# Kernel optimization log

Measured on AMD Instinct MI355X. Metric: run time of the kernel, lower is better.

Reference implementation:

```python
import jax, jax.numpy as jnp
import numpy as np

B, T, U, N, K, H, O = 64, 800, 64, 64, 10, 512, 121
CLIP_LSTM, CLIP_OUT = 10.0, 100.0


def setup_inputs() -> dict:
    key = jax.random.key(0)
    ks = jax.random.split(key, 16)
    s = 0.08
    return {
        "strokes": jax.random.normal(ks[0], (B, T, 3), jnp.float32),
        "transcriptions": jax.random.uniform(ks[1], (B, U, N), jnp.float32),
        "W0": jax.random.normal(ks[2], (3 + N, 4 * H), jnp.float32) * s,
        "R0": jax.random.normal(ks[3], (H, 4 * H), jnp.float32) * s,
        "b0": jnp.zeros((4 * H,), jnp.float32),
        "Wd": jax.random.normal(ks[4], (H, 3 * K), jnp.float32) * 0.01,
        "bd": jnp.zeros((3 * K,), jnp.float32),
        "W1": jax.random.normal(ks[5], (H + N + 3, 4 * H), jnp.float32) * s,
        "R1": jax.random.normal(ks[6], (H, 4 * H), jnp.float32) * s,
        "b1": jnp.zeros((4 * H,), jnp.float32),
        "W2": jax.random.normal(ks[7], (H + N + 3, 4 * H), jnp.float32) * s,
        "R2": jax.random.normal(ks[8], (H, 4 * H), jnp.float32) * s,
        "b2": jnp.zeros((4 * H,), jnp.float32),
        "Wo": jax.random.normal(ks[9], (3 * H, O), jnp.float32) * s,
        "bo": jnp.zeros((O,), jnp.float32),
    }


def _lstm_step(h, c, z):
    i, f, g, o = jnp.split(z, 4, axis=-1)
    c2 = jax.nn.sigmoid(f) * c + jax.nn.sigmoid(i) * jnp.tanh(g)
    h2 = jax.nn.sigmoid(o) * jnp.tanh(c2)
    return h2, c2


def _lstm_layer(x_seq, W, R, b):
    # x_seq: [T, B, D] -> hidden sequence [T, B, H]
    xz = jnp.einsum('tbd,dh->tbh', x_seq, W) + b  # precompute input projections

    def step(carry, xz_t):
        h, c = carry
        h2, c2 = _lstm_step(h, c, xz_t + h @ R)
        return (h2, c2), h2

    z0 = jnp.zeros((x_seq.shape[1], R.shape[0]), x_seq.dtype)
    _, hs = jax.lax.scan(step, (z0, z0), xz)
    return hs


def _make_clipper(cv):
    @jax.custom_vjp
    def f(y):
        return y
    f.defvjp(lambda y: (y, None), lambda _, dy: (jnp.clip(dy, -cv, cv),))
    return f


_clip_lstm = _make_clipper(CLIP_LSTM)
_clip_out = _make_clipper(CLIP_OUT)


def _forward(strokes, transcriptions, W0, R0, b0, Wd, bd, W1, R1, b1, W2, R2, b2, Wo, bo):
    idx = jnp.arange(1, U + 2, dtype=strokes.dtype)  # enumerated char positions [U+1]
    x_t = jnp.swapaxes(strokes, 0, 1)  # [T, B, 3]

    def step(carry, x):
        w, kappa, h, c = carry
        z = jnp.concatenate([x, w], axis=-1) @ W0 + h @ R0 + b0
        h2, c2 = _lstm_step(h, c, z)
        y = jnp.exp(h2 @ Wd + bd).reshape(-1, 3, K)  # [B, 3, K]
        alpha, beta, dk = y[:, 0], y[:, 1], y[:, 2]
        kappa2 = kappa + dk  # [B, K]
        # Gaussian window over U+1 positions, summed over K mixtures
        phi = alpha[..., None] * jnp.exp(-beta[..., None] * (kappa2[..., None] - idx) ** 2)
        wfull = phi.sum(axis=1)  # [B, U+1]
        att = jnp.argmax(wfull, axis=-1).astype(strokes.dtype)  # [B]
        w2 = jnp.einsum('bu,bun->bn', wfull[:, :U], transcriptions)  # soft window [B, N]
        return (w2, kappa2, h2, c2), (h2, w2, att)

    zf = lambda d: jnp.zeros((B, d), strokes.dtype)
    init = (zf(N), zf(K), zf(H), zf(H))
    _, (h0_seq, w_seq, att_seq) = jax.lax.scan(step, init, x_t)

    x1 = jnp.concatenate([_clip_lstm(h0_seq), w_seq, x_t], axis=-1)  # [T, B, H+N+3]
    h1_seq = _lstm_layer(x1, W1, R1, b1)
    x2 = jnp.concatenate([_clip_lstm(h1_seq), w_seq, x_t], axis=-1)
    h2_seq = _lstm_layer(x2, W2, R2, b2)
    hall = jnp.concatenate([h0_seq, h1_seq, h2_seq], axis=-1)  # [T, B, 3H]
    out = _clip_out(hall @ Wo + bo)
    return jnp.swapaxes(out, 0, 1), jnp.swapaxes(att_seq, 0, 1)  # [B,T,O], [B,T]


def reference(strokes, transcriptions, W0, R0, b0, Wd, bd, W1, R1, b1, W2, R2, b2, Wo, bo):
    return _forward(strokes, transcriptions, W0, R0, b0, Wd, bd, W1, R1, b1, W2, R2, b2, Wo, bo)
```

## Files before the change

### kernel.cpp

```cpp
#include <hip/hip_runtime.h>

#define B_   64
#define T_   800
#define U_   64
#define N_   64
#define KMIX 10
#define H_   512
#define O_   121
#define C4_  2048

#define NB_L0  64
#define NB_L1  64
#define NB_L2  64
#define NB_OUT 8
#define NB_ATT 4
#define NBLK  (NB_L0 + NB_L1 + NB_L2 + NB_OUT + NB_ATT)
#define NTHR  512
#define RING  8
#define RB    (RING - 1)
#define FS    8

#define AL(pp) __hip_atomic_load((pp), __ATOMIC_RELAXED, __HIP_MEMORY_SCOPE_AGENT)

struct Params {
  const float* strokes; const float* transcr;
  const float* W0; const float* b0;
  const float* bd;
  const float* W1; const float* b1;
  const float* W2; const float* b2;
  const float* bo;
  const float4* PR0; const float4* PW0w;
  const float4* PH1; const float4* PR1; const float4* PW1w;
  const float4* PH2; const float4* PR2; const float4* PW2w;
  const float4* PWo; const float4* PWd;
  float* h0r; float* h1r; float* h2r;
  float* wr;
  int *h0f, *h1f, *h2f, *wfl, *outf;
  float* outp; float* attp;
};

__device__ __forceinline__ float sigf(float x) { return 1.0f / (1.0f + expf(-x)); }

__device__ __forceinline__ double f32q(double x) {
  double ax = fabs(x);
  if (ax >= 0x1p-126) return (double)(float)x;
  return rint(x * 0x1p149) * 0x1p-149;
}

__device__ __forceinline__ void cstoref(float* p, float v) {
  __hip_atomic_store(p, v, __ATOMIC_RELAXED, __HIP_MEMORY_SCOPE_AGENT);
}

__device__ __forceinline__ int* FP(int* arr, int tt, int bq) {
  return arr + ((size_t)tt * 8 + bq) * FS;
}
__device__ __forceinline__ void waitflag(const int* f, int target) {
  while (__hip_atomic_load(f, __ATOMIC_RELAXED, __HIP_MEMORY_SCOPE_AGENT) < target)
    __builtin_amdgcn_s_sleep(1);
}
__device__ __forceinline__ void postflag(int* f) {
  __hip_atomic_fetch_add(f, 1, __ATOMIC_RELAXED, __HIP_MEMORY_SCOPE_AGENT);
}

__device__ __forceinline__ void stage4k(float* dstL, const float* src, int t) {
  const double* s = (const double*)src;
  double v0 = AL(s + t), v1 = AL(s + 512 + t), v2 = AL(s + 1024 + t), v3 = AL(s + 1536 + t);
  double* d = (double*)dstL;
  d[t] = v0; d[512 + t] = v1; d[1024 + t] = v2; d[1536 + t] = v3;
}
__device__ __forceinline__ void stage4k2(float* d1, const float* s1,
                                         float* d2, const float* s2, int t) {
  const double* a = (const double*)s1;
  const double* b = (const double*)s2;
  double a0 = AL(a + t), a1 = AL(a + 512 + t), a2 = AL(a + 1024 + t), a3 = AL(a + 1536 + t);
  double b0 = AL(b + t), b1 = AL(b + 512 + t), b2 = AL(b + 1024 + t), b3 = AL(b + 1536 + t);
  double* dA = (double*)d1; dA[t] = a0; dA[512 + t] = a1; dA[1024 + t] = a2; dA[1536 + t] = a3;
  double* dB = (double*)d2; dB[t] = b0; dB[512 + t] = b1; dB[1024 + t] = b2; dB[1536 + t] = b3;
}
__device__ __forceinline__ void stage512(float* dstL, const float* src, int t) {
  if (t < 256) {
    double v = AL((const double*)src + t);
    ((double*)dstL)[t] = v;
  }
}

__device__ __forceinline__ void dot4gl(const float* Xl,
                                       const float4* __restrict__ W,
                                       int k4, int col, float acc[4]) {
  const float4* X = (const float4*)Xl;
  #pragma unroll 2
  for (int kk = 0; kk < k4; ++kk) {
    float4 xv = X[kk];
    #pragma unroll
    for (int g = 0; g < 4; ++g) {
      float4 wv = W[kk * C4_ + g * H_ + col];
      acc[g] = fmaf(xv.x, wv.x, acc[g]);
      acc[g] = fmaf(xv.y, wv.y, acc[g]);
      acc[g] = fmaf(xv.z, wv.z, acc[g]);
      acc[g] = fmaf(xv.w, wv.w, acc[g]);
    }
  }
}

__device__ __forceinline__ float dot1l(const float* Xl,
                                       const float4* __restrict__ W,
                                       int k4, int stride) {
  const float4* X = (const float4*)Xl;
  float a = 0.0f;
  #pragma unroll 4
  for (int kk = 0; kk < k4; ++kk) {
    float4 xv = X[kk];
    float4 wv = W[kk * stride];
    a = fmaf(xv.x, wv.x, a); a = fmaf(xv.y, wv.y, a);
    a = fmaf(xv.z, wv.z, a); a = fmaf(xv.w, wv.w, a);
  }
  return a;
}

__global__ void pack_k(const float* __restrict__ src, float* __restrict__ dst,
                       int K, int C, int ld) {
  int idx = blockIdx.x * 256 + threadIdx.x;
  if (idx >= K * C) return;
  int k = idx / C, c = idx - k * C;
  dst[(size_t)(k >> 2) * C * 4 + (size_t)c * 4 + (k & 3)] = src[(size_t)k * ld + c];
}

__global__ __launch_bounds__(NTHR, 2)
void net_kernel(Params p) {
  const int q = blockIdx.x;
  const int t = threadIdx.x;

  __shared__ float  s_buf[12288];
  __shared__ float  s_y[16][32];
  __shared__ float  s_k2[16][10];
  __shared__ float  s_kap[16][10];
  __shared__ double s_wf[16][66];

  if (q < NB_L0) {
    const int bq = q >> 3, colg = q & 7;
    const int bl = t >> 6, cl = t & 63;
    const int b = bq * 8 + bl, col = colg * 64 + cl;
    float* sh = s_buf;
    float* sw = s_buf + 4096;
    float creg = 0.0f;
    for (int i = 0; i < T_; ++i) {
      if (t == 0) {
        if (i >= 1) waitflag(FP(p.h0f, i - 1, bq), 8);
        if (i >= 8) waitflag(FP(p.outf, i - 8, bq), 1);
      }
      __syncthreads();
      const int slp = (i - 1) & RB;
      stage4k(sh, &p.h0r[((size_t)slp * B_ + bq * 8) * H_], t);
      float acc[4];
      const float* xs = &p.strokes[(b * T_ + i) * 3];
      float x0 = xs[0], x1 = xs[1], x2 = xs[2];
      #pragma unroll
      for (int g = 0; g < 4; ++g) {
        int cg = g * H_ + col;
        acc[g] = p.b0[cg] + x0 * p.W0[cg] + x1 * p.W0[C4_ + cg] + x2 * p.W0[2 * C4_ + cg];
      }
      __syncthreads();
      dot4gl(sh + bl * H_, p.PR0, H_ / 4, col, acc);
      if (t == 0 && i >= 1) waitflag(FP(p.wfl, i - 1, bq), 1);
      __syncthreads();
      stage512(sw, &p.wr[((size_t)slp * B_ + bq * 8) * N_], t);
      __syncthreads();
      dot4gl(sw + bl * N_, p.PW0w, N_ / 4, col, acc);
      float cn = sigf(acc[1]) * creg + sigf(acc[0]) * tanhf(acc[2]);
      float hn = sigf(acc[3]) * tanhf(cn);
      creg = cn;
      cstoref(&p.h0r[((size_t)(i & RB) * B_ + b) * H_ + col], hn);
      __syncthreads();
      if (t == 0) postflag(FP(p.h0f, i, bq));
    }
  } else if (q < NB_L0 + NB_L1) {
    const int qq = q - NB_L0;
    const int bq = qq >> 3, colg = qq & 7;
    const int bl = t >> 6, cl = t & 63;
    const int b = bq * 8 + bl, col = colg * 64 + cl;
    float* sh0 = s_buf;
    float* sh1 = s_buf + 4096;
    float* sw  = s_buf + 8192;
    float creg = 0.0f;
    for (int tt = 0; tt < T_; ++tt) {
      if (t == 0) {
        waitflag(FP(p.h0f, tt, bq), 8);
        if (tt >= 1) waitflag(FP(p.h1f, tt - 1, bq), 8);
        if (tt >= 7) waitflag(FP(p.outf, tt - 7, bq), 1);
      }
      __syncthreads();
      const int sl = tt & RB, slp = (tt - 1) & RB;
      stage4k2(sh0, &p.h0r[((size_t)sl * B_ + bq * 8) * H_],
               sh1, &p.h1r[((size_t)slp * B_ + bq * 8) * H_], t);
      float acc[4];
      const float* xs = &p.strokes[(b * T_ + tt) * 3];
      float x0 = xs[0], x1 = xs[1], x2 = xs[2];
      #pragma unroll
      for (int g = 0; g < 4; ++g) {
        int cg = g * H_ + col;
        acc[g] = p.b1[cg] + x0 * p.W1[576 * C4_ + cg] + x1 * p.W1[577 * C4_ + cg]
                          + x2 * p.W1[578 * C4_ + cg];
      }
      __syncthreads();
      dot4gl(sh0 + bl * H_, p.PH1, H_ / 4, col, acc);
      dot4gl(sh1 + bl * H_, p.PR1, H_ / 4, col, acc);
      if (t == 0) waitflag(FP(p.wfl, tt, bq), 1);
      __syncthreads();
      stage512(sw, &p.wr[((size_t)sl * B_ + bq * 8) * N_], t);
      __syncthreads();
      dot4gl(sw + bl * N_, p.PW1w, N_ / 4, col, acc);
      float cn = sigf(acc[1]) * creg + sigf(acc[0]) * tanhf(acc[2]);
      float hn = sigf(acc[3]) * tanhf(cn);
      creg = cn;
      cstoref(&p.h1r[((size_t)sl * B_ + b) * H_ + col], hn);
      __syncthreads();
      if (t == 0) postflag(FP(p.h1f, tt, bq));
    }
  } else if (q < NB_L0 + NB_L1 + NB_L2) {
    const int qq = q - NB_L0 - NB_L1;
    const int bq = qq >> 3, colg = qq & 7;
    const int bl = t >> 6, cl = t & 63;
    const int b = bq * 8 + bl, col = colg * 64 + cl;
    float* sh1 = s_buf;
    float* sh2 = s_buf + 4096;
    float* sw  = s_buf + 8192;
    float creg = 0.0f;
    for (int tt = 0; tt < T_; ++tt) {
      if (t == 0) {
        waitflag(FP(p.h1f, tt, bq), 8);
        waitflag(FP(p.wfl, tt, bq), 1);
        if (tt >= 1) waitflag(FP(p.h2f, tt - 1, bq), 8);
        if (tt >= 6) waitflag(FP(p.outf, tt - 6, bq), 1);
      }
      __syncthreads();
      const int sl = tt & RB, slp = (tt - 1) & RB;
      stage4k2(sh1, &p.h1r[((size_t)sl * B_ + bq * 8) * H_],
               sh2, &p.h2r[((size_t)slp * B_ + bq * 8) * H_], t);
      stage512(sw, &p.wr[((size_t)sl * B_ + bq * 8) * N_], t);
      float acc[4];
      const float* xs = &p.strokes[(b * T_ + tt) * 3];
      float x0 = xs[0], x1 = xs[1], x2 = xs[2];
      #pragma unroll
      for (int g = 0; g < 4; ++g) {
        int cg = g * H_ + col;
        acc[g] = p.b2[cg] + x0 * p.W2[576 * C4_ + cg] + x1 * p.W2[577 * C4_ + cg]
                          + x2 * p.W2[578 * C4_ + cg];
      }
      __syncthreads();
      dot4gl(sh1 + bl * H_, p.PH2, H_ / 4, col, acc);
      dot4gl(sw + bl * N_, p.PW2w, N_ / 4, col, acc);
      dot4gl(sh2 + bl * H_, p.PR2, H_ / 4, col, acc);
      float cn = sigf(acc[1]) * creg + sigf(acc[0]) * tanhf(acc[2]);
      float hn = sigf(acc[3]) * tanhf(cn);
      creg = cn;
      cstoref(&p.h2r[((size_t)sl * B_ + b) * H_ + col], hn);
      __syncthreads();
      if (t == 0) postflag(FP(p.h2f, tt, bq));
    }
  } else if (q < NB_L0 + NB_L1 + NB_L2 + NB_OUT) {
    const int bq = q - NB_L0 - NB_L1 - NB_L2;
    const int bl = t >> 6, ol = t & 63;
    const int b = bq * 8 + bl;
    const int oo1 = ol;
    const bool v2 = (ol < O_ - 64);
    const int oo2 = v2 ? (ol + 64) : 0;
    float* sx0 = s_buf;
    float* sx1 = s_buf + 4096;
    float* sx2 = s_buf + 8192;
    for (int tt = 0; tt < T_; ++tt) {
      if (t == 0) {
        waitflag(FP(p.h0f, tt, bq), 8);
        waitflag(FP(p.h1f, tt, bq), 8);
        waitflag(FP(p.h2f, tt, bq), 8);
      }
      __syncthreads();
      const int sl = tt & RB;
      {
        const double* a = (const double*)&p.h0r[((size_t)sl * B_ + bq * 8) * H_];
        const double* c = (const double*)&p.h1r[((size_t)sl * B_ + bq * 8) * H_];
        const double* e = (const double*)&p.h2r[((size_t)sl * B_ + bq * 8) * H_];
        double a0 = AL(a + t), a1 = AL(a + 512 + t), a2 = AL(a + 1024 + t), a3 = AL(a + 1536 + t);
        double c0 = AL(c + t), c1 = AL(c + 512 + t), c2 = AL(c + 1024 + t), c3 = AL(c + 1536 + t);
        double e0 = AL(e + t), e1 = AL(e + 512 + t), e2 = AL(e + 1024 + t), e3 = AL(e + 1536 + t);
        double* dA = (double*)sx0; dA[t] = a0; dA[512 + t] = a1; dA[1024 + t] = a2; dA[1536 + t] = a3;
        double* dC = (double*)sx1; dC[t] = c0; dC[512 + t] = c1; dC[1024 + t] = c2; dC[1536 + t] = c3;
        double* dE = (double*)sx2; dE[t] = e0; dE[512 + t] = e1; dE[1024 + t] = e2; dE[1536 + t] = e3;
      }
      __syncthreads();
      const float* X0 = sx0 + bl * H_;
      const float* X1 = sx1 + bl * H_;
      const float* X2 = sx2 + bl * H_;
      float a1v = p.bo[oo1];
      a1v += dot1l(X0, p.PWo + oo1, 128, O_);
      a1v += dot1l(X1, p.PWo + (size_t)128 * O_ + oo1, 128, O_);
      a1v += dot1l(X2, p.PWo + (size_t)256 * O_ + oo1, 128, O_);
      float a2v = p.bo[oo2];
      a2v += dot1l(X0, p.PWo + oo2, 128, O_);
      a2v += dot1l(X1, p.PWo + (size_t)128 * O_ + oo2, 128, O_);
      a2v += dot1l(X2, p.PWo + (size_t)256 * O_ + oo2, 128, O_);
      __builtin_nontemporal_store(a1v, &p.outp[(size_t)(b * T_ + tt) * O_ + oo1]);
      if (v2) __builtin_nontemporal_store(a2v, &p.outp[(size_t)(b * T_ + tt) * O_ + oo2]);
      __syncthreads();
      if (t == 0) postflag(FP(p.outf, tt, bq));
    }
  } else {
    const int qa = q - NB_L0 - NB_L1 - NB_L2 - NB_OUT;
    const int lb = t >> 5, s = t & 31;
    const int ub = qa * 16 + lb;
    for (int z = t; z < 160; z += NTHR) ((float*)s_kap)[z] = 0.0f;
    __syncthreads();
    for (int tt = 0; tt < T_; ++tt) {
      if (t == 0) {
        waitflag(FP(p.h0f, tt, 2 * qa), 8);
        waitflag(FP(p.h0f, tt, 2 * qa + 1), 8);
      }
      __syncthreads();
      const int sl = tt & RB;
      {
        const double* sA = (const double*)&p.h0r[((size_t)sl * B_ + qa * 16) * H_];
        double v[8];
        #pragma unroll
        for (int k = 0; k < 8; ++k) v[k] = AL(sA + k * 512 + t);
        double* d = (double*)s_buf;
        #pragma unroll
        for (int k = 0; k < 8; ++k) d[k * 512 + t] = v[k];
      }
      __syncthreads();
      if (s < 30) {
        float a = p.bd[s] + dot1l(s_buf + lb * H_, p.PWd + s, 128, 30);
        float y = expf(a);
        s_y[lb][s] = y;
        if (s >= 20) {
          float k2 = s_kap[lb][s - 20] + y;
          s_kap[lb][s - 20] = k2;
          s_k2[lb][s - 20] = k2;
        }
      }
      __syncthreads();
      for (int u = s; u < U_ + 1; u += 32) {
        double wf = 0.0;
        #pragma unroll
        for (int k = 0; k < KMIX; ++k) {
          float d32 = s_k2[lb][k] - (float)(u + 1);
          float sq  = d32 * d32;
          float m   = -(s_y[lb][10 + k] * sq);
          double e  = exp((double)m);
          double e32 = (e < 0x1p-126) ? 0.0 : (double)(float)e;
          wf += f32q((double)s_y[lb][k] * e32);
        }
        s_wf[lb][u] = wf;
      }
      __syncthreads();
      if (s == 0) {
        int am = 0; double bv = s_wf[lb][0];
        for (int u = 1; u < U_ + 1; ++u) {
          double v = s_wf[lb][u];
          if (v > bv) { bv = v; am = u; }
        }
        __builtin_nontemporal_store((float)am, &p.attp[ub * T_ + tt]);
      }
      for (int n = s; n < N_; n += 32) {
        float a2 = 0.f;
        for (int u = 0; u < U_; ++u)
          a2 = fmaf((float)s_wf[lb][u], p.transcr[(size_t)(ub * U_ + u) * N_ + n], a2);
        cstoref(&p.wr[((size_t)sl * B_ + ub) * N_ + n], a2);
      }
      __syncthreads();
      if (t == 0) {
        postflag(FP(p.wfl, tt, 2 * qa));
        postflag(FP(p.wfl, tt, 2 * qa + 1));
      }
    }
  }
}

extern "C" void kernel_launch(void* const* d_in, const int* in_sizes, int n_in,
                              void* d_out, int out_size, void* d_ws, size_t ws_size,
                              hipStream_t stream) {
  (void)in_sizes; (void)n_in; (void)out_size; (void)ws_size;
  const float* strokes = (const float*)d_in[0];
  const float* transcr = (const float*)d_in[1];
  const float* W0 = (const float*)d_in[2];
  const float* R0 = (const float*)d_in[3];
  const float* b0 = (const float*)d_in[4];
  const float* Wd = (const float*)d_in[5];
  const float* bd = (const float*)d_in[6];
  const float* W1 = (const float*)d_in[7];
  const float* R1 = (const float*)d_in[8];
  const float* b1 = (const float*)d_in[9];
  const float* W2 = (const float*)d_in[10];
  const float* R2 = (const float*)d_in[11];
  const float* b2 = (const float*)d_in[12];
  const float* Wo = (const float*)d_in[13];
  const float* bo = (const float*)d_in[14];

  float* ws = (float*)d_ws;
  size_t off = 0;
  float* h0r = ws + off; off += (size_t)RING * B_ * H_;
  float* h1r = ws + off; off += (size_t)RING * B_ * H_;
  float* h2r = ws + off; off += (size_t)RING * B_ * H_;
  float* wr  = ws + off; off += (size_t)RING * B_ * N_;
  const size_t FLAGN = (size_t)T_ * 8 * FS;
  int* h0f  = (int*)(ws + off); off += FLAGN;
  int* h1f  = (int*)(ws + off); off += FLAGN;
  int* h2f  = (int*)(ws + off); off += FLAGN;
  int* wfl  = (int*)(ws + off); off += FLAGN;
  int* outf = (int*)(ws + off); off += FLAGN;
  size_t stateFloats = off;
  float* PR0  = ws + off; off += (size_t)512 * 2048;
  float* PW0w = ws + off; off += (size_t)64 * 2048;
  float* PH1  = ws + off; off += (size_t)512 * 2048;
  float* PR1  = ws + off; off += (size_t)512 * 2048;
  float* PW1w = ws + off; off += (size_t)64 * 2048;
  float* PH2  = ws + off; off += (size_t)512 * 2048;
  float* PR2  = ws + off; off += (size_t)512 * 2048;
  float* PW2w = ws + off; off += (size_t)64 * 2048;
  float* PWo  = ws + off; off += (size_t)1536 * 121;
  float* PWd  = ws + off; off += (size_t)512 * 30;

  (void)hipMemsetAsync(d_ws, 0, stateFloats * sizeof(float), stream);

  auto packl = [&](const float* src, float* dst, int K, int C, int ld) {
    int n = K * C;
    pack_k<<<dim3((n + 255) / 256), dim3(256), 0, stream>>>(src, dst, K, C, ld);
  };
  packl(R0, PR0, 512, 2048, 2048);
  packl(W0 + 3 * 2048, PW0w, 64, 2048, 2048);
  packl(W1, PH1, 512, 2048, 2048);
  packl(R1, PR1, 512, 2048, 2048);
  packl(W1 + 512 * 2048, PW1w, 64, 2048, 2048);
  packl(W2, PH2, 512, 2048, 2048);
  packl(R2, PR2, 512, 2048, 2048);
  packl(W2 + 512 * 2048, PW2w, 64, 2048, 2048);
  packl(Wo, PWo, 1536, 121, 121);
  packl(Wd, PWd, 512, 30, 30);

  Params p;
  p.strokes = strokes; p.transcr = transcr;
  p.W0 = W0; p.b0 = b0; p.bd = bd;
  p.W1 = W1; p.b1 = b1; p.W2 = W2; p.b2 = b2; p.bo = bo;
  p.PR0 = (const float4*)PR0; p.PW0w = (const float4*)PW0w;
  p.PH1 = (const float4*)PH1; p.PR1 = (const float4*)PR1; p.PW1w = (const float4*)PW1w;
  p.PH2 = (const float4*)PH2; p.PR2 = (const float4*)PR2; p.PW2w = (const float4*)PW2w;
  p.PWo = (const float4*)PWo; p.PWd = (const float4*)PWd;
  p.h0r = h0r; p.h1r = h1r; p.h2r = h2r; p.wr = wr;
  p.h0f = h0f; p.h1f = h1f; p.h2f = h2f; p.wfl = wfl; p.outf = outf;
  p.outp = (float*)d_out;
  p.attp = (float*)d_out + (size_t)B_ * T_ * O_;

  void* args[] = { (void*)&p };
  (void)hipLaunchCooperativeKernel((const void*)net_kernel, dim3(NBLK), dim3(NTHR),
                                   args, 0, stream);
}
```

Baseline: 56.15 ms.

## Repack LSTM weights gate-interleaved, use packed FMA, and reorder recurrent dependency waits

```diff
diff --git a/kernel.cpp b/kernel.cpp
--- a/kernel.cpp
+++ b/kernel.cpp
@@ -16,11 +16,13 @@
 #define NB_ATT 4
 #define NBLK  (NB_L0 + NB_L1 + NB_L2 + NB_OUT + NB_ATT)
 #define NTHR  512
-#define RING  8
+#define RING  16
 #define RB    (RING - 1)
 #define FS    8
 
 #define AL(pp) __hip_atomic_load((pp), __ATOMIC_RELAXED, __HIP_MEMORY_SCOPE_AGENT)
+
+typedef float pk2 __attribute__((ext_vector_type(2)));
 
 struct Params {
   const float* strokes; const float* transcr;
@@ -68,15 +70,6 @@
   double* d = (double*)dstL;
   d[t] = v0; d[512 + t] = v1; d[1024 + t] = v2; d[1536 + t] = v3;
 }
-__device__ __forceinline__ void stage4k2(float* d1, const float* s1,
-                                         float* d2, const float* s2, int t) {
-  const double* a = (const double*)s1;
-  const double* b = (const double*)s2;
-  double a0 = AL(a + t), a1 = AL(a + 512 + t), a2 = AL(a + 1024 + t), a3 = AL(a + 1536 + t);
-  double b0 = AL(b + t), b1 = AL(b + 512 + t), b2 = AL(b + 1024 + t), b3 = AL(b + 1536 + t);
-  double* dA = (double*)d1; dA[t] = a0; dA[512 + t] = a1; dA[1024 + t] = a2; dA[1536 + t] = a3;
-  double* dB = (double*)d2; dB[t] = b0; dB[512 + t] = b1; dB[1024 + t] = b2; dB[1536 + t] = b3;
-}
 __device__ __forceinline__ void stage512(float* dstL, const float* src, int t) {
   if (t < 256) {
     double v = AL((const double*)src + t);
@@ -84,21 +77,24 @@
   }
 }
 
-__device__ __forceinline__ void dot4gl(const float* Xl,
-                                       const float4* __restrict__ W,
-                                       int k4, int col, float acc[4]) {
+__device__ __forceinline__ pk2 mk2(float a, float b) { pk2 r; r.x = a; r.y = b; return r; }
+
+__device__ __forceinline__ void dot4g(const float* Xl, const float4* __restrict__ Wu,
+                                      int k4, pk2& a01, pk2& a23) {
   const float4* X = (const float4*)Xl;
-  #pragma unroll 2
+  #pragma unroll 4
   for (int kk = 0; kk < k4; ++kk) {
     float4 xv = X[kk];
-    #pragma unroll
-    for (int g = 0; g < 4; ++g) {
-      float4 wv = W[kk * C4_ + g * H_ + col];
-      acc[g] = fmaf(xv.x, wv.x, acc[g]);
-      acc[g] = fmaf(xv.y, wv.y, acc[g]);
-      acc[g] = fmaf(xv.z, wv.z, acc[g]);
-      acc[g] = fmaf(xv.w, wv.w, acc[g]);
-    }
+    const float4* wp = Wu + (size_t)kk * (H_ * 4);
+    float4 w0 = wp[0], w1 = wp[1], w2 = wp[2], w3 = wp[3];
+    a01 = __builtin_elementwise_fma(mk2(w0.x, w0.y), mk2(xv.x, xv.x), a01);
+    a23 = __builtin_elementwise_fma(mk2(w0.z, w0.w), mk2(xv.x, xv.x), a23);
+    a01 = __builtin_elementwise_fma(mk2(w1.x, w1.y), mk2(xv.y, xv.y), a01);
+    a23 = __builtin_elementwise_fma(mk2(w1.z, w1.w), mk2(xv.y, xv.y), a23);
+    a01 = __builtin_elementwise_fma(mk2(w2.x, w2.y), mk2(xv.z, xv.z), a01);
+    a23 = __builtin_elementwise_fma(mk2(w2.z, w2.w), mk2(xv.z, xv.z), a23);
+    a01 = __builtin_elementwise_fma(mk2(w3.x, w3.y), mk2(xv.w, xv.w), a01);
+    a23 = __builtin_elementwise_fma(mk2(w3.z, w3.w), mk2(xv.w, xv.w), a23);
   }
 }
 
@@ -125,6 +121,17 @@
   dst[(size_t)(k >> 2) * C * 4 + (size_t)c * 4 + (k & 3)] = src[(size_t)k * ld + c];
 }
 
+__global__ void pack_kg(const float* __restrict__ src, float* __restrict__ dst,
+                        int K, int ld) {
+  int idx = blockIdx.x * 256 + threadIdx.x;
+  if (idx >= K * C4_) return;
+  int k = idx >> 11;
+  int g = (idx >> 9) & 3;
+  int u = idx & 511;
+  dst[((size_t)(k >> 2) * H_ + u) * 16 + (size_t)(k & 3) * 4 + g] =
+      src[(size_t)k * ld + g * H_ + u];
+}
+
 __global__ __launch_bounds__(NTHR, 2)
 void net_kernel(Params p) {
   const int q = blockIdx.x;
@@ -138,122 +145,143 @@
 
   if (q < NB_L0) {
     const int bq = q >> 3, colg = q & 7;
-    const int bl = t >> 6, cl = t & 63;
-    const int b = bq * 8 + bl, col = colg * 64 + cl;
+    const int bl = t >> 6;
+    const int u = colg * 64 + (t & 63);
+    const int b = bq * 8 + bl;
     float* sh = s_buf;
     float* sw = s_buf + 4096;
+    const float4* WuR = p.PR0 + (size_t)u * 4;
+    const float4* WuW = p.PW0w + (size_t)u * 4;
     float creg = 0.0f;
     for (int i = 0; i < T_; ++i) {
       if (t == 0) {
         if (i >= 1) waitflag(FP(p.h0f, i - 1, bq), 8);
-        if (i >= 8) waitflag(FP(p.outf, i - 8, bq), 1);
+        if (i >= RING) waitflag(FP(p.outf, i - RING, bq), 1);
       }
       __syncthreads();
       const int slp = (i - 1) & RB;
       stage4k(sh, &p.h0r[((size_t)slp * B_ + bq * 8) * H_], t);
-      float acc[4];
-      const float* xs = &p.strokes[(b * T_ + i) * 3];
-      float x0 = xs[0], x1 = xs[1], x2 = xs[2];
-      #pragma unroll
-      for (int g = 0; g < 4; ++g) {
-        int cg = g * H_ + col;
-        acc[g] = p.b0[cg] + x0 * p.W0[cg] + x1 * p.W0[C4_ + cg] + x2 * p.W0[2 * C4_ + cg];
-      }
-      __syncthreads();
-      dot4gl(sh + bl * H_, p.PR0, H_ / 4, col, acc);
+      pk2 a01, a23;
+      {
+        const float* xs = &p.strokes[(b * T_ + i) * 3];
+        float x0 = xs[0], x1 = xs[1], x2 = xs[2];
+        int c0 = u, c1 = H_ + u, c2 = 2 * H_ + u, c3 = 3 * H_ + u;
+        a01.x = p.b0[c0] + x0 * p.W0[c0] + x1 * p.W0[C4_ + c0] + x2 * p.W0[2 * C4_ + c0];
+        a01.y = p.b0[c1] + x0 * p.W0[c1] + x1 * p.W0[C4_ + c1] + x2 * p.W0[2 * C4_ + c1];
+        a23.x = p.b0[c2] + x0 * p.W0[c2] + x1 * p.W0[C4_ + c2] + x2 * p.W0[2 * C4_ + c2];
+        a23.y = p.b0[c3] + x0 * p.W0[c3] + x1 * p.W0[C4_ + c3] + x2 * p.W0[2 * C4_ + c3];
+      }
+      __syncthreads();
+      dot4g(sh + bl * H_, WuR, H_ / 4, a01, a23);
       if (t == 0 && i >= 1) waitflag(FP(p.wfl, i - 1, bq), 1);
       __syncthreads();
       stage512(sw, &p.wr[((size_t)slp * B_ + bq * 8) * N_], t);
       __syncthreads();
-      dot4gl(sw + bl * N_, p.PW0w, N_ / 4, col, acc);
-      float cn = sigf(acc[1]) * creg + sigf(acc[0]) * tanhf(acc[2]);
-      float hn = sigf(acc[3]) * tanhf(cn);
+      dot4g(sw + bl * N_, WuW, N_ / 4, a01, a23);
+      float cn = sigf(a01.y) * creg + sigf(a01.x) * tanhf(a23.x);
+      float hn = sigf(a23.y) * tanhf(cn);
       creg = cn;
-      cstoref(&p.h0r[((size_t)(i & RB) * B_ + b) * H_ + col], hn);
+      cstoref(&p.h0r[((size_t)(i & RB) * B_ + b) * H_ + u], hn);
       __syncthreads();
       if (t == 0) postflag(FP(p.h0f, i, bq));
     }
   } else if (q < NB_L0 + NB_L1) {
     const int qq = q - NB_L0;
     const int bq = qq >> 3, colg = qq & 7;
-    const int bl = t >> 6, cl = t & 63;
-    const int b = bq * 8 + bl, col = colg * 64 + cl;
+    const int bl = t >> 6;
+    const int u = colg * 64 + (t & 63);
+    const int b = bq * 8 + bl;
     float* sh0 = s_buf;
     float* sh1 = s_buf + 4096;
     float* sw  = s_buf + 8192;
+    const float4* WuH = p.PH1 + (size_t)u * 4;
+    const float4* WuR = p.PR1 + (size_t)u * 4;
+    const float4* WuW = p.PW1w + (size_t)u * 4;
     float creg = 0.0f;
     for (int tt = 0; tt < T_; ++tt) {
       if (t == 0) {
-        waitflag(FP(p.h0f, tt, bq), 8);
         if (tt >= 1) waitflag(FP(p.h1f, tt - 1, bq), 8);
-        if (tt >= 7) waitflag(FP(p.outf, tt - 7, bq), 1);
+        if (tt >= RING - 1) waitflag(FP(p.outf, tt - (RING - 1), bq), 1);
       }
       __syncthreads();
       const int sl = tt & RB, slp = (tt - 1) & RB;
-      stage4k2(sh0, &p.h0r[((size_t)sl * B_ + bq * 8) * H_],
-               sh1, &p.h1r[((size_t)slp * B_ + bq * 8) * H_], t);
-      float acc[4];
-      const float* xs = &p.strokes[(b * T_ + tt) * 3];
-      float x0 = xs[0], x1 = xs[1], x2 = xs[2];
-      #pragma unroll
-      for (int g = 0; g < 4; ++g) {
-        int cg = g * H_ + col;
-        acc[g] = p.b1[cg] + x0 * p.W1[576 * C4_ + cg] + x1 * p.W1[577 * C4_ + cg]
-                          + x2 * p.W1[578 * C4_ + cg];
-      }
-      __syncthreads();
-      dot4gl(sh0 + bl * H_, p.PH1, H_ / 4, col, acc);
-      dot4gl(sh1 + bl * H_, p.PR1, H_ / 4, col, acc);
+      stage4k(sh1, &p.h1r[((size_t)slp * B_ + bq * 8) * H_], t);
+      pk2 a01, a23;
+      {
+        const float* xs = &p.strokes[(b * T_ + tt) * 3];
+        float x0 = xs[0], x1 = xs[1], x2 = xs[2];
+        int c0 = u, c1 = H_ + u, c2 = 2 * H_ + u, c3 = 3 * H_ + u;
+        a01.x = p.b1[c0] + x0 * p.W1[576 * C4_ + c0] + x1 * p.W1[577 * C4_ + c0] + x2 * p.W1[578 * C4_ + c0];
+        a01.y = p.b1[c1] + x0 * p.W1[576 * C4_ + c1] + x1 * p.W1[577 * C4_ + c1] + x2 * p.W1[578 * C4_ + c1];
+        a23.x = p.b1[c2] + x0 * p.W1[576 * C4_ + c2] + x1 * p.W1[577 * C4_ + c2] + x2 * p.W1[578 * C4_ + c2];
+        a23.y = p.b1[c3] + x0 * p.W1[576 * C4_ + c3] + x1 * p.W1[577 * C4_ + c3] + x2 * p.W1[578 * C4_ + c3];
+      }
+      __syncthreads();
+      dot4g(sh1 + bl * H_, WuR, H_ / 4, a01, a23);
+      if (t == 0) waitflag(FP(p.h0f, tt, bq), 8);
+      __syncthreads();
+      stage4k(sh0, &p.h0r[((size_t)sl * B_ + bq * 8) * H_], t);
+      __syncthreads();
+      dot4g(sh0 + bl * H_, WuH, H_ / 4, a01, a23);
       if (t == 0) waitflag(FP(p.wfl, tt, bq), 1);
       __syncthreads();
       stage512(sw, &p.wr[((size_t)sl * B_ + bq * 8) * N_], t);
       __syncthreads();
-      dot4gl(sw + bl * N_, p.PW1w, N_ / 4, col, acc);
-      float cn = sigf(acc[1]) * creg + sigf(acc[0]) * tanhf(acc[2]);
-      float hn = sigf(acc[3]) * tanhf(cn);
+      dot4g(sw + bl * N_, WuW, N_ / 4, a01, a23);
+      float cn = sigf(a01.y) * creg + sigf(a01.x) * tanhf(a23.x);
+      float hn = sigf(a23.y) * tanhf(cn);
       creg = cn;
-      cstoref(&p.h1r[((size_t)sl * B_ + b) * H_ + col], hn);
+      cstoref(&p.h1r[((size_t)sl * B_ + b) * H_ + u], hn);
       __syncthreads();
       if (t == 0) postflag(FP(p.h1f, tt, bq));
     }
   } else if (q < NB_L0 + NB_L1 + NB_L2) {
     const int qq = q - NB_L0 - NB_L1;
     const int bq = qq >> 3, colg = qq & 7;
-    const int bl = t >> 6, cl = t & 63;
-    const int b = bq * 8 + bl, col = colg * 64 + cl;
+    const int bl = t >> 6;
+    const int u = colg * 64 + (t & 63);
+    const int b = bq * 8 + bl;
     float* sh1 = s_buf;
     float* sh2 = s_buf + 4096;
     float* sw  = s_buf + 8192;
+    const float4* WuH = p.PH2 + (size_t)u * 4;
+    const float4* WuR = p.PR2 + (size_t)u * 4;
+    const float4* WuW = p.PW2w + (size_t)u * 4;
     float creg = 0.0f;
     for (int tt = 0; tt < T_; ++tt) {
       if (t == 0) {
-        waitflag(FP(p.h1f, tt, bq), 8);
-        waitflag(FP(p.wfl, tt, bq), 1);
         if (tt >= 1) waitflag(FP(p.h2f, tt - 1, bq), 8);
-        if (tt >= 6) waitflag(FP(p.outf, tt - 6, bq), 1);
+        if (tt >= RING - 2) waitflag(FP(p.outf, tt - (RING - 2), bq), 1);
       }
       __syncthreads();
       const int sl = tt & RB, slp = (tt - 1) & RB;
-      stage4k2(sh1, &p.h1r[((size_t)sl * B_ + bq * 8) * H_],
-               sh2, &p.h2r[((size_t)slp * B_ + bq * 8) * H_], t);
+      stage4k(sh2, &p.h2r[((size_t)slp * B_ + bq * 8) * H_], t);
+      pk2 a01, a23;
+      {
+        const float* xs = &p.strokes[(b * T_ + tt) * 3];
+        float x0 = xs[0], x1 = xs[1], x2 = xs[2];
+        int c0 = u, c1 = H_ + u, c2 = 2 * H_ + u, c3 = 3 * H_ + u;
+        a01.x = p.b2[c0] + x0 * p.W2[576 * C4_ + c0] + x1 * p.W2[577 * C4_ + c0] + x2 * p.W2[578 * C4_ + c0];
+        a01.y = p.b2[c1] + x0 * p.W2[576 * C4_ + c1] + x1 * p.W2[577 * C4_ + c1] + x2 * p.W2[578 * C4_ + c1];
+        a23.x = p.b2[c2] + x0 * p.W2[576 * C4_ + c2] + x1 * p.W2[577 * C4_ + c2] + x2 * p.W2[578 * C4_ + c2];
+        a23.y = p.b2[c3] + x0 * p.W2[576 * C4_ + c3] + x1 * p.W2[577 * C4_ + c3] + x2 * p.W2[578 * C4_ + c3];
+      }
+      __syncthreads();
+      dot4g(sh2 + bl * H_, WuR, H_ / 4, a01, a23);
+      if (t == 0) waitflag(FP(p.h1f, tt, bq), 8);
+      __syncthreads();
+      stage4k(sh1, &p.h1r[((size_t)sl * B_ + bq * 8) * H_], t);
+      __syncthreads();
+      dot4g(sh1 + bl * H_, WuH, H_ / 4, a01, a23);
+      if (t == 0) waitflag(FP(p.wfl, tt, bq), 1);
+      __syncthreads();
       stage512(sw, &p.wr[((size_t)sl * B_ + bq * 8) * N_], t);
-      float acc[4];
-      const float* xs = &p.strokes[(b * T_ + tt) * 3];
-      float x0 = xs[0], x1 = xs[1], x2 = xs[2];
-      #pragma unroll
-      for (int g = 0; g < 4; ++g) {
-        int cg = g * H_ + col;
-        acc[g] = p.b2[cg] + x0 * p.W2[576 * C4_ + cg] + x1 * p.W2[577 * C4_ + cg]
-                          + x2 * p.W2[578 * C4_ + cg];
-      }
-      __syncthreads();
-      dot4gl(sh1 + bl * H_, p.PH2, H_ / 4, col, acc);
-      dot4gl(sw + bl * N_, p.PW2w, N_ / 4, col, acc);
-      dot4gl(sh2 + bl * H_, p.PR2, H_ / 4, col, acc);
-      float cn = sigf(acc[1]) * creg + sigf(acc[0]) * tanhf(acc[2]);
-      float hn = sigf(acc[3]) * tanhf(cn);
+      __syncthreads();
+      dot4g(sw + bl * N_, WuW, N_ / 4, a01, a23);
+      float cn = sigf(a01.y) * creg + sigf(a01.x) * tanhf(a23.x);
+      float hn = sigf(a23.y) * tanhf(cn);
       creg = cn;
-      cstoref(&p.h2r[((size_t)sl * B_ + b) * H_ + col], hn);
+      cstoref(&p.h2r[((size_t)sl * B_ + b) * H_ + u], hn);
       __syncthreads();
       if (t == 0) postflag(FP(p.h2f, tt, bq));
     }
@@ -424,14 +452,18 @@
     int n = K * C;
     pack_k<<<dim3((n + 255) / 256), dim3(256), 0, stream>>>(src, dst, K, C, ld);
   };
-  packl(R0, PR0, 512, 2048, 2048);
-  packl(W0 + 3 * 2048, PW0w, 64, 2048, 2048);
-  packl(W1, PH1, 512, 2048, 2048);
-  packl(R1, PR1, 512, 2048, 2048);
-  packl(W1 + 512 * 2048, PW1w, 64, 2048, 2048);
-  packl(W2, PH2, 512, 2048, 2048);
-  packl(R2, PR2, 512, 2048, 2048);
-  packl(W2 + 512 * 2048, PW2w, 64, 2048, 2048);
+  auto packg = [&](const float* src, float* dst, int K) {
+    int n = K * C4_;
+    pack_kg<<<dim3((n + 255) / 256), dim3(256), 0, stream>>>(src, dst, K, C4_);
+  };
+  packg(R0, PR0, 512);
+  packg(W0 + 3 * 2048, PW0w, 64);
+  packg(W1, PH1, 512);
+  packg(R1, PR1, 512);
+  packg(W1 + 512 * 2048, PW1w, 64);
+  packg(W2, PH2, 512);
+  packg(R2, PR2, 512);
+  packg(W2 + 512 * 2048, PW2w, 64);
   packl(Wo, PWo, 1536, 121, 121);
   packl(Wd, PWd, 512, 30, 30);
 
```

After: 100.3 ms. 78.6% more time.

## Split-K the recurrent LSTM and output dot products across 1024-thread blocks

Applied to the files above, without the earlier changes.

```diff
diff --git a/kernel.cpp b/kernel.cpp
--- a/kernel.cpp
+++ b/kernel.cpp
@@ -15,7 +15,7 @@
 #define NB_OUT 8
 #define NB_ATT 4
 #define NBLK  (NB_L0 + NB_L1 + NB_L2 + NB_OUT + NB_ATT)
-#define NTHR  512
+#define NTHR  1024
 #define RING  8
 #define RB    (RING - 1)
 #define FS    8
@@ -64,18 +64,18 @@
 
 __device__ __forceinline__ void stage4k(float* dstL, const float* src, int t) {
   const double* s = (const double*)src;
-  double v0 = AL(s + t), v1 = AL(s + 512 + t), v2 = AL(s + 1024 + t), v3 = AL(s + 1536 + t);
+  double v0 = AL(s + t), v1 = AL(s + 1024 + t);
   double* d = (double*)dstL;
-  d[t] = v0; d[512 + t] = v1; d[1024 + t] = v2; d[1536 + t] = v3;
+  d[t] = v0; d[1024 + t] = v1;
 }
 __device__ __forceinline__ void stage4k2(float* d1, const float* s1,
                                          float* d2, const float* s2, int t) {
   const double* a = (const double*)s1;
   const double* b = (const double*)s2;
-  double a0 = AL(a + t), a1 = AL(a + 512 + t), a2 = AL(a + 1024 + t), a3 = AL(a + 1536 + t);
-  double b0 = AL(b + t), b1 = AL(b + 512 + t), b2 = AL(b + 1024 + t), b3 = AL(b + 1536 + t);
-  double* dA = (double*)d1; dA[t] = a0; dA[512 + t] = a1; dA[1024 + t] = a2; dA[1536 + t] = a3;
-  double* dB = (double*)d2; dB[t] = b0; dB[512 + t] = b1; dB[1024 + t] = b2; dB[1536 + t] = b3;
+  double a0 = AL(a + t), a1 = AL(a + 1024 + t);
+  double b0 = AL(b + t), b1 = AL(b + 1024 + t);
+  double* dA = (double*)d1; dA[t] = a0; dA[1024 + t] = a1;
+  double* dB = (double*)d2; dB[t] = b0; dB[1024 + t] = b1;
 }
 __device__ __forceinline__ void stage512(float* dstL, const float* src, int t) {
   if (t < 256) {
@@ -125,7 +125,7 @@
   dst[(size_t)(k >> 2) * C * 4 + (size_t)c * 4 + (k & 3)] = src[(size_t)k * ld + c];
 }
 
-__global__ __launch_bounds__(NTHR, 2)
+__global__ __launch_bounds__(NTHR, 4)
 void net_kernel(Params p) {
   const int q = blockIdx.x;
   const int t = threadIdx.x;
@@ -138,10 +138,12 @@
 
   if (q < NB_L0) {
     const int bq = q >> 3, colg = q & 7;
-    const int bl = t >> 6, cl = t & 63;
+    const int kh = t >> 9;
+    const int bl = (t >> 6) & 7, cl = t & 63;
     const int b = bq * 8 + bl, col = colg * 64 + cl;
     float* sh = s_buf;
     float* sw = s_buf + 4096;
+    float4* s_red = (float4*)(s_buf + 4608);
     float creg = 0.0f;
     for (int i = 0; i < T_; ++i) {
       if (t == 0) {
@@ -151,36 +153,45 @@
       __syncthreads();
       const int slp = (i - 1) & RB;
       stage4k(sh, &p.h0r[((size_t)slp * B_ + bq * 8) * H_], t);
-      float acc[4];
-      const float* xs = &p.strokes[(b * T_ + i) * 3];
-      float x0 = xs[0], x1 = xs[1], x2 = xs[2];
-      #pragma unroll
-      for (int g = 0; g < 4; ++g) {
-        int cg = g * H_ + col;
-        acc[g] = p.b0[cg] + x0 * p.W0[cg] + x1 * p.W0[C4_ + cg] + x2 * p.W0[2 * C4_ + cg];
-      }
-      __syncthreads();
-      dot4gl(sh + bl * H_, p.PR0, H_ / 4, col, acc);
+      float acc[4] = {0.f, 0.f, 0.f, 0.f};
+      if (kh == 0) {
+        const float* xs = &p.strokes[(b * T_ + i) * 3];
+        float x0 = xs[0], x1 = xs[1], x2 = xs[2];
+        #pragma unroll
+        for (int g = 0; g < 4; ++g) {
+          int cg = g * H_ + col;
+          acc[g] = p.b0[cg] + x0 * p.W0[cg] + x1 * p.W0[C4_ + cg] + x2 * p.W0[2 * C4_ + cg];
+        }
+      }
+      __syncthreads();
+      dot4gl(sh + bl * H_ + kh * 256, p.PR0 + (size_t)kh * 64 * C4_, 64, col, acc);
       if (t == 0 && i >= 1) waitflag(FP(p.wfl, i - 1, bq), 1);
       __syncthreads();
       stage512(sw, &p.wr[((size_t)slp * B_ + bq * 8) * N_], t);
       __syncthreads();
-      dot4gl(sw + bl * N_, p.PW0w, N_ / 4, col, acc);
-      float cn = sigf(acc[1]) * creg + sigf(acc[0]) * tanhf(acc[2]);
-      float hn = sigf(acc[3]) * tanhf(cn);
-      creg = cn;
-      cstoref(&p.h0r[((size_t)(i & RB) * B_ + b) * H_ + col], hn);
+      dot4gl(sw + bl * N_ + kh * 32, p.PW0w + (size_t)kh * 8 * C4_, 8, col, acc);
+      if (kh) { float4 r; r.x = acc[0]; r.y = acc[1]; r.z = acc[2]; r.w = acc[3]; s_red[t - 512] = r; }
+      __syncthreads();
+      if (!kh) {
+        float4 r = s_red[t];
+        float cn = sigf(acc[1] + r.y) * creg + sigf(acc[0] + r.x) * tanhf(acc[2] + r.z);
+        float hn = sigf(acc[3] + r.w) * tanhf(cn);
+        creg = cn;
+        cstoref(&p.h0r[((size_t)(i & RB) * B_ + b) * H_ + col], hn);
+      }
       __syncthreads();
       if (t == 0) postflag(FP(p.h0f, i, bq));
     }
   } else if (q < NB_L0 + NB_L1) {
     const int qq = q - NB_L0;
     const int bq = qq >> 3, colg = qq & 7;
-    const int bl = t >> 6, cl = t & 63;
+    const int kh = t >> 9;
+    const int bl = (t >> 6) & 7, cl = t & 63;
     const int b = bq * 8 + bl, col = colg * 64 + cl;
     float* sh0 = s_buf;
     float* sh1 = s_buf + 4096;
     float* sw  = s_buf + 8192;
+    float4* s_red = (float4*)(s_buf + 8704);
     float creg = 0.0f;
     for (int tt = 0; tt < T_; ++tt) {
       if (t == 0) {
@@ -192,38 +203,47 @@
       const int sl = tt & RB, slp = (tt - 1) & RB;
       stage4k2(sh0, &p.h0r[((size_t)sl * B_ + bq * 8) * H_],
                sh1, &p.h1r[((size_t)slp * B_ + bq * 8) * H_], t);
-      float acc[4];
-      const float* xs = &p.strokes[(b * T_ + tt) * 3];
-      float x0 = xs[0], x1 = xs[1], x2 = xs[2];
-      #pragma unroll
-      for (int g = 0; g < 4; ++g) {
-        int cg = g * H_ + col;
-        acc[g] = p.b1[cg] + x0 * p.W1[576 * C4_ + cg] + x1 * p.W1[577 * C4_ + cg]
-                          + x2 * p.W1[578 * C4_ + cg];
-      }
-      __syncthreads();
-      dot4gl(sh0 + bl * H_, p.PH1, H_ / 4, col, acc);
-      dot4gl(sh1 + bl * H_, p.PR1, H_ / 4, col, acc);
+      float acc[4] = {0.f, 0.f, 0.f, 0.f};
+      if (kh == 0) {
+        const float* xs = &p.strokes[(b * T_ + tt) * 3];
+        float x0 = xs[0], x1 = xs[1], x2 = xs[2];
+        #pragma unroll
+        for (int g = 0; g < 4; ++g) {
+          int cg = g * H_ + col;
+          acc[g] = p.b1[cg] + x0 * p.W1[576 * C4_ + cg] + x1 * p.W1[577 * C4_ + cg]
+                            + x2 * p.W1[578 * C4_ + cg];
+        }
+      }
+      __syncthreads();
+      dot4gl(sh0 + bl * H_ + kh * 256, p.PH1 + (size_t)kh * 64 * C4_, 64, col, acc);
+      dot4gl(sh1 + bl * H_ + kh * 256, p.PR1 + (size_t)kh * 64 * C4_, 64, col, acc);
       if (t == 0) waitflag(FP(p.wfl, tt, bq), 1);
       __syncthreads();
       stage512(sw, &p.wr[((size_t)sl * B_ + bq * 8) * N_], t);
       __syncthreads();
-      dot4gl(sw + bl * N_, p.PW1w, N_ / 4, col, acc);
-      float cn = sigf(acc[1]) * creg + sigf(acc[0]) * tanhf(acc[2]);
-      float hn = sigf(acc[3]) * tanhf(cn);
-      creg = cn;
-      cstoref(&p.h1r[((size_t)sl * B_ + b) * H_ + col], hn);
+      dot4gl(sw + bl * N_ + kh * 32, p.PW1w + (size_t)kh * 8 * C4_, 8, col, acc);
+      if (kh) { float4 r; r.x = acc[0]; r.y = acc[1]; r.z = acc[2]; r.w = acc[3]; s_red[t - 512] = r; }
+      __syncthreads();
+      if (!kh) {
+        float4 r = s_red[t];
+        float cn = sigf(acc[1] + r.y) * creg + sigf(acc[0] + r.x) * tanhf(acc[2] + r.z);
+        float hn = sigf(acc[3] + r.w) * tanhf(cn);
+        creg = cn;
+        cstoref(&p.h1r[((size_t)sl * B_ + b) * H_ + col], hn);
+      }
       __syncthreads();
       if (t == 0) postflag(FP(p.h1f, tt, bq));
     }
   } else if (q < NB_L0 + NB_L1 + NB_L2) {
     const int qq = q - NB_L0 - NB_L1;
     const int bq = qq >> 3, colg = qq & 7;
-    const int bl = t >> 6, cl = t & 63;
+    const int kh = t >> 9;
+    const int bl = (t >> 6) & 7, cl = t & 63;
     const int b = bq * 8 + bl, col = colg * 64 + cl;
     float* sh1 = s_buf;
     float* sh2 = s_buf + 4096;
     float* sw  = s_buf + 8192;
+    float4* s_red = (float4*)(s_buf + 8704);
     float creg = 0.0f;
     for (int tt = 0; tt < T_; ++tt) {
       if (t == 0) {
@@ -237,29 +257,37 @@
       stage4k2(sh1, &p.h1r[((size_t)sl * B_ + bq * 8) * H_],
                sh2, &p.h2r[((size_t)slp * B_ + bq * 8) * H_], t);
       stage512(sw, &p.wr[((size_t)sl * B_ + bq * 8) * N_], t);
-      float acc[4];
-      const float* xs = &p.strokes[(b * T_ + tt) * 3];
-      float x0 = xs[0], x1 = xs[1], x2 = xs[2];
-      #pragma unroll
-      for (int g = 0; g < 4; ++g) {
-        int cg = g * H_ + col;
-        acc[g] = p.b2[cg] + x0 * p.W2[576 * C4_ + cg] + x1 * p.W2[577 * C4_ + cg]
-                          + x2 * p.W2[578 * C4_ + cg];
-      }
-      __syncthreads();
-      dot4gl(sh1 + bl * H_, p.PH2, H_ / 4, col, acc);
-      dot4gl(sw + bl * N_, p.PW2w, N_ / 4, col, acc);
-      dot4gl(sh2 + bl * H_, p.PR2, H_ / 4, col, acc);
-      float cn = sigf(acc[1]) * creg + sigf(acc[0]) * tanhf(acc[2]);
-      float hn = sigf(acc[3]) * tanhf(cn);
-      creg = cn;
-      cstoref(&p.h2r[((size_t)sl * B_ + b) * H_ + col], hn);
+      float acc[4] = {0.f, 0.f, 0.f, 0.f};
+      if (kh == 0) {
+        const float* xs = &p.strokes[(b * T_ + tt) * 3];
+        float x0 = xs[0], x1 = xs[1], x2 = xs[2];
+        #pragma unroll
+        for (int g = 0; g < 4; ++g) {
+          int cg = g * H_ + col;
+          acc[g] = p.b2[cg] + x0 * p.W2[576 * C4_ + cg] + x1 * p.W2[577 * C4_ + cg]
+                            + x2 * p.W2[578 * C4_ + cg];
+        }
+      }
+      __syncthreads();
+      dot4gl(sh1 + bl * H_ + kh * 256, p.PH2 + (size_t)kh * 64 * C4_, 64, col, acc);
+      dot4gl(sw + bl * N_ + kh * 32, p.PW2w + (size_t)kh * 8 * C4_, 8, col, acc);
+      dot4gl(sh2 + bl * H_ + kh * 256, p.PR2 + (size_t)kh * 64 * C4_, 64, col, acc);
+      if (kh) { float4 r; r.x = acc[0]; r.y = acc[1]; r.z = acc[2]; r.w = acc[3]; s_red[t - 512] = r; }
+      __syncthreads();
+      if (!kh) {
+        float4 r = s_red[t];
+        float cn = sigf(acc[1] + r.y) * creg + sigf(acc[0] + r.x) * tanhf(acc[2] + r.z);
+        float hn = sigf(acc[3] + r.w) * tanhf(cn);
+        creg = cn;
+        cstoref(&p.h2r[((size_t)sl * B_ + b) * H_ + col], hn);
+      }
       __syncthreads();
       if (t == 0) postflag(FP(p.h2f, tt, bq));
     }
   } else if (q < NB_L0 + NB_L1 + NB_L2 + NB_OUT) {
     const int bq = q - NB_L0 - NB_L1 - NB_L2;
-    const int bl = t >> 6, ol = t & 63;
+    const int kh = t >> 9;
+    const int bl = (t >> 6) & 7, ol = t & 63;
     const int b = bq * 8 + bl;
     const int oo1 = ol;
     const bool v2 = (ol < O_ - 64);
@@ -267,6 +295,7 @@
     float* sx0 = s_buf;
     float* sx1 = s_buf + 4096;
     float* sx2 = s_buf + 8192;
+    float* s_red = (float*)s_wf;
     for (int tt = 0; tt < T_; ++tt) {
       if (t == 0) {
         waitflag(FP(p.h0f, tt, bq), 8);
@@ -279,27 +308,34 @@
         const double* a = (const double*)&p.h0r[((size_t)sl * B_ + bq * 8) * H_];
         const double* c = (const double*)&p.h1r[((size_t)sl * B_ + bq * 8) * H_];
         const double* e = (const double*)&p.h2r[((size_t)sl * B_ + bq * 8) * H_];
-        double a0 = AL(a + t), a1 = AL(a + 512 + t), a2 = AL(a + 1024 + t), a3 = AL(a + 1536 + t);
-        double c0 = AL(c + t), c1 = AL(c + 512 + t), c2 = AL(c + 1024 + t), c3 = AL(c + 1536 + t);
-        double e0 = AL(e + t), e1 = AL(e + 512 + t), e2 = AL(e + 1024 + t), e3 = AL(e + 1536 + t);
-        double* dA = (double*)sx0; dA[t] = a0; dA[512 + t] = a1; dA[1024 + t] = a2; dA[1536 + t] = a3;
-        double* dC = (double*)sx1; dC[t] = c0; dC[512 + t] = c1; dC[1024 + t] = c2; dC[1536 + t] = c3;
-        double* dE = (double*)sx2; dE[t] = e0; dE[512 + t] = e1; dE[1024 + t] = e2; dE[1536 + t] = e3;
-      }
-      __syncthreads();
-      const float* X0 = sx0 + bl * H_;
-      const float* X1 = sx1 + bl * H_;
-      const float* X2 = sx2 + bl * H_;
-      float a1v = p.bo[oo1];
-      a1v += dot1l(X0, p.PWo + oo1, 128, O_);
-      a1v += dot1l(X1, p.PWo + (size_t)128 * O_ + oo1, 128, O_);
-      a1v += dot1l(X2, p.PWo + (size_t)256 * O_ + oo1, 128, O_);
-      float a2v = p.bo[oo2];
-      a2v += dot1l(X0, p.PWo + oo2, 128, O_);
-      a2v += dot1l(X1, p.PWo + (size_t)128 * O_ + oo2, 128, O_);
-      a2v += dot1l(X2, p.PWo + (size_t)256 * O_ + oo2, 128, O_);
-      __builtin_nontemporal_store(a1v, &p.outp[(size_t)(b * T_ + tt) * O_ + oo1]);
-      if (v2) __builtin_nontemporal_store(a2v, &p.outp[(size_t)(b * T_ + tt) * O_ + oo2]);
+        double a0 = AL(a + t), a1 = AL(a + 1024 + t);
+        double c0 = AL(c + t), c1 = AL(c + 1024 + t);
+        double e0 = AL(e + t), e1 = AL(e + 1024 + t);
+        double* dA = (double*)sx0; dA[t] = a0; dA[1024 + t] = a1;
+        double* dC = (double*)sx1; dC[t] = c0; dC[1024 + t] = c1;
+        double* dE = (double*)sx2; dE[t] = e0; dE[1024 + t] = e1;
+      }
+      __syncthreads();
+      const float* X0 = sx0 + bl * H_ + kh * 256;
+      const float* X1 = sx1 + bl * H_ + kh * 256;
+      const float* X2 = sx2 + bl * H_ + kh * 256;
+      const size_t khO = (size_t)(kh * 64) * O_;
+      float a1v = kh ? 0.0f : p.bo[oo1];
+      a1v += dot1l(X0, p.PWo + khO + oo1, 64, O_);
+      a1v += dot1l(X1, p.PWo + (size_t)128 * O_ + khO + oo1, 64, O_);
+      a1v += dot1l(X2, p.PWo + (size_t)256 * O_ + khO + oo1, 64, O_);
+      float a2v = kh ? 0.0f : p.bo[oo2];
+      a2v += dot1l(X0, p.PWo + khO + oo2, 64, O_);
+      a2v += dot1l(X1, p.PWo + (size_t)128 * O_ + khO + oo2, 64, O_);
+      a2v += dot1l(X2, p.PWo + (size_t)256 * O_ + khO + oo2, 64, O_);
+      if (kh) { s_red[(t - 512) * 2] = a1v; s_red[(t - 512) * 2 + 1] = a2v; }
+      __syncthreads();
+      if (!kh) {
+        a1v += s_red[t * 2];
+        a2v += s_red[t * 2 + 1];
+        __builtin_nontemporal_store(a1v, &p.outp[(size_t)(b * T_ + tt) * O_ + oo1]);
+        if (v2) __builtin_nontemporal_store(a2v, &p.outp[(size_t)(b * T_ + tt) * O_ + oo2]);
+      }
       __syncthreads();
       if (t == 0) postflag(FP(p.outf, tt, bq));
     }
@@ -318,15 +354,15 @@
       const int sl = tt & RB;
       {
         const double* sA = (const double*)&p.h0r[((size_t)sl * B_ + qa * 16) * H_];
-        double v[8];
+        double v[4];
         #pragma unroll
-        for (int k = 0; k < 8; ++k) v[k] = AL(sA + k * 512 + t);
+        for (int k = 0; k < 4; ++k) v[k] = AL(sA + k * 1024 + t);
         double* d = (double*)s_buf;
         #pragma unroll
-        for (int k = 0; k < 8; ++k) d[k * 512 + t] = v[k];
-      }
-      __syncthreads();
-      if (s < 30) {
+        for (int k = 0; k < 4; ++k) d[k * 1024 + t] = v[k];
+      }
+      __syncthreads();
+      if (t < 512 && s < 30) {
         float a = p.bd[s] + dot1l(s_buf + lb * H_, p.PWd + s, 128, 30);
         float y = expf(a);
         s_y[lb][s] = y;
@@ -337,21 +373,23 @@
         }
       }
       __syncthreads();
-      for (int u = s; u < U_ + 1; u += 32) {
-        double wf = 0.0;
-        #pragma unroll
-        for (int k = 0; k < KMIX; ++k) {
-          float d32 = s_k2[lb][k] - (float)(u + 1);
-          float sq  = d32 * d32;
-          float m   = -(s_y[lb][10 + k] * sq);
-          double e  = exp((double)m);
-          double e32 = (e < 0x1p-126) ? 0.0 : (double)(float)e;
-          wf += f32q((double)s_y[lb][k] * e32);
-        }
-        s_wf[lb][u] = wf;
-      }
-      __syncthreads();
-      if (s == 0) {
+      if (t < 512) {
+        for (int u = s; u < U_ + 1; u += 32) {
+          double wf = 0.0;
+          #pragma unroll
+          for (int k = 0; k < KMIX; ++k) {
+            float d32 = s_k2[lb][k] - (float)(u + 1);
+            float sq  = d32 * d32;
+            float m   = -(s_y[lb][10 + k] * sq);
+            double e  = exp((double)m);
+            double e32 = (e < 0x1p-126) ? 0.0 : (double)(float)e;
+            wf += f32q((double)s_y[lb][k] * e32);
+          }
+          s_wf[lb][u] = wf;
+        }
+      }
+      __syncthreads();
+      if (t < 512 && s == 0) {
         int am = 0; double bv = s_wf[lb][0];
         for (int u = 1; u < U_ + 1; ++u) {
           double v = s_wf[lb][u];
@@ -359,11 +397,13 @@
         }
         __builtin_nontemporal_store((float)am, &p.attp[ub * T_ + tt]);
       }
-      for (int n = s; n < N_; n += 32) {
-        float a2 = 0.f;
-        for (int u = 0; u < U_; ++u)
-          a2 = fmaf((float)s_wf[lb][u], p.transcr[(size_t)(ub * U_ + u) * N_ + n], a2);
-        cstoref(&p.wr[((size_t)sl * B_ + ub) * N_ + n], a2);
+      if (t < 512) {
+        for (int n = s; n < N_; n += 32) {
+          float a2 = 0.f;
+          for (int u = 0; u < U_; ++u)
+            a2 = fmaf((float)s_wf[lb][u], p.transcr[(size_t)(ub * U_ + u) * N_ + n], a2);
+          cstoref(&p.wr[((size_t)sl * B_ + ub) * N_ + n], a2);
+        }
       }
       __syncthreads();
       if (t == 0) {
```

Result: faster. 52.89 ms (-5.8%).
